# Performance work log

Hardware: AMD Instinct MI355X
Metric: run time of the kernel (lower is better)

## Reference

```python
import jax, jax.numpy as jnp
from jax import lax
import numpy as np


def _conv(x, w, b, groups=1):
    # x: NCHW, w: OIHW, stride 1, SAME padding
    y = lax.conv_general_dilated(x, w, (1, 1), 'SAME',
                                 dimension_numbers=('NCHW', 'OIHW', 'NCHW'),
                                 feature_group_count=groups)
    return y + b[None, :, None, None]


def setup_inputs() -> dict:
    key = jax.random.key(0)
    ks = jax.random.split(key, 9)
    B, C, H, W, N, K = 8, 64, 256, 256, 10, 64
    f = lambda k, s, sc=0.05: jax.random.normal(k, s, dtype=jnp.float32) * sc
    return dict(
        x=jax.random.normal(ks[0], (B, C, H, W), dtype=jnp.float32),
        ln_g=jnp.ones((C,), jnp.float32), ln_b=jnp.zeros((C,), jnp.float32),
        conv3_w=f(ks[1], (C, C, 3, 3)), conv3_b=jnp.zeros((C,), jnp.float32),
        dw_w=f(ks[2], (C, 1, 3, 3)), dw_b=jnp.zeros((C,), jnp.float32),
        c1_w=f(ks[3], (C, C, 1, 1)), c1_b=jnp.zeros((C,), jnp.float32),
        c2_w=f(ks[4], (N, C, 1, 1)), c2_b=jnp.zeros((N,), jnp.float32),
        base=f(ks[5], (N, K, K), 1.0),
        up_w=f(ks[6], (K, C, 3, 3)), up_b=jnp.zeros((K,), jnp.float32),
        down_w=f(ks[7], (C, K, 3, 3)), down_b=jnp.zeros((C,), jnp.float32),
    )


def reference(x, ln_g, ln_b, conv3_w, conv3_b, dw_w, dw_b, c1_w, c1_b,
              c2_w, c2_b, base, up_w, up_b, down_w, down_b):
    eps = 1e-5
    # LayerNorm over channel dim (permute(0,2,3,1) -> LN(last) -> permute back)
    mu = jnp.mean(x, axis=1, keepdims=True)
    var = jnp.var(x, axis=1, keepdims=True)
    xn = (x - mu) / jnp.sqrt(var + eps) * ln_g[None, :, None, None] + ln_b[None, :, None, None]
    x1 = jax.nn.gelu(_conv(xn, conv3_w, conv3_b), approximate=False)
    # predict module: dwconv -> GAP -> 1x1 -> relu -> 1x1 -> softmax over N
    C = x.shape[1]
    p = _conv(x1, dw_w, dw_b, groups=C)
    p = jnp.mean(p, axis=(2, 3), keepdims=True)           # [B,C,1,1]
    p = jax.nn.relu(_conv(p, c1_w, c1_b))
    p = _conv(p, c2_w, c2_b)[:, :, 0, 0]                  # [B,N]
    w = jax.nn.softmax(p, axis=1)                         # [B,N]
    # blend N basis KxK matrices per sample
    Wm = jnp.einsum('bn,nkl->bkl', w, base)               # [B,K,K]
    xm = _conv(x1, up_w, up_b)                            # [B,K,H,W]
    B, K, H, Wd = xm.shape
    xm = jnp.einsum('bkl,bkm->blm', Wm, xm.reshape(B, K, H * Wd)).reshape(B, K, H, Wd)
    xm = _conv(xm, down_w, down_b)                        # [B,C,H,W]
    return x + xm
```

## Files before the change

kernel.cpp:

```cpp
#include <hip/hip_runtime.h>
#include <math.h>

constexpr int B = 8, C = 64, H = 256, W = 256, HWc = H * W, N = 10;

typedef short bf8 __attribute__((ext_vector_type(8)));
typedef float f4  __attribute__((ext_vector_type(4)));
typedef unsigned short ushort;

__device__ __forceinline__ ushort f2bf(float f) {
  unsigned u = __builtin_bit_cast(unsigned, f);
  unsigned r = (u + 0x7fffu + ((u >> 16) & 1u)) >> 16;
  return (ushort)r;
}
__device__ __forceinline__ float bf2f(ushort h) {
  unsigned u = ((unsigned)h) << 16;
  return __builtin_bit_cast(float, u);
}

__global__ __launch_bounds__(256) void ln_k(
    const float* __restrict__ x, const float* __restrict__ g,
    const float* __restrict__ bt, ushort* __restrict__ xn) {
  int pix = blockIdx.x * 256 + threadIdx.x;
  int b = blockIdx.y;
  const float* xp = x + (size_t)b * C * HWc + pix;
  float v[64];
  float s = 0.f, s2 = 0.f;
#pragma unroll
  for (int c = 0; c < 64; c++) {
    v[c] = xp[(size_t)c * HWc];
    s += v[c]; s2 += v[c] * v[c];
  }
  float mu = s * (1.f / 64);
  float var = s2 * (1.f / 64) - mu * mu;
  float rstd = rsqrtf(var + 1e-5f);
  ushort* op = xn + ((size_t)b * HWc + pix) * 64;
#pragma unroll
  for (int ch = 0; ch < 8; ch++) {
    union { ushort us[8]; int4 v4; } pk;
#pragma unroll
    for (int j = 0; j < 8; j++) {
      int c = ch * 8 + j;
      pk.us[j] = f2bf((v[c] - mu) * rstd * g[c] + bt[c]);
    }
    *reinterpret_cast<int4*>(op + ch * 8) = pk.v4;
  }
}

__global__ void prep_w(const float* __restrict__ w3, const float* __restrict__ wu,
                       const float* __restrict__ wd, ushort* __restrict__ frags) {
  int idx = blockIdx.x * 256 + threadIdx.x;
  if (idx >= 3 * 4608) return;
  int conv = idx / 4608, r = idx % 4608;
  int s = r >> 8, cf = (r >> 6) & 3, lane = r & 63;
  const float* w = (conv == 0) ? w3 : (conv == 1) ? wu : wd;
  int co = (cf << 4) + (lane & 15);
  int tap = s >> 1;
  ushort* o = frags + conv * 36864 + ((size_t)r) * 8;
#pragma unroll
  for (int j = 0; j < 8; j++) {
    int ci = ((s & 1) << 5) + ((lane >> 4) << 3) + j;
    o[j] = f2bf(w[(co * 64 + ci) * 9 + tap]);
  }
}

typedef __attribute__((address_space(3))) unsigned lds_u32;
typedef __attribute__((address_space(1))) const unsigned glb_u32;

__device__ __forceinline__ void stage_gll(
    char* ldsbuf, const ushort* __restrict__ in, const ushort* __restrict__ zbuf,
    int b, int h0, int w0, int ch2, int tid) {
  int wave = tid >> 6, lane = tid & 63;
#pragma unroll
  for (int it = 0; it < 6; it++) {
    int idx = it * 256 + wave * 64 + lane;
    int pix = idx >> 2, ch = idx & 3;
    int r = pix / 18, c = pix % 18;
    int gh = h0 + r - 1, gw = w0 + c - 1;
    int chs = ch ^ ((c >> 1) & 3);
    bool ok = (idx < 1296) && (gh >= 0) && (gh < H) && (gw >= 0) && (gw < W);
    const ushort* src = ok
        ? in + (((size_t)b * H + gh) * W + gw) * 64 + ch2 * 32 + chs * 8
        : zbuf;
    char* dst = ldsbuf + (it * 256 + wave * 64) * 16;
    __builtin_amdgcn_global_load_lds((glb_u32*)(const void*)src,
                                     (lds_u32*)(void*)dst, 16, 0, 0);
  }
}

__device__ __forceinline__ void compute_half(
    const char* lds, const bf8* __restrict__ wf, int ch2,
    int wave, int lm, int lk, f4 (&acc)[16]) {
#pragma unroll
  for (int dx = 0; dx < 3; dx++) {
    bf8 wb3[3];
#pragma unroll
    for (int dy = 0; dy < 3; dy++) {
      int s = ((dy * 3 + dx) << 1) | ch2;
      wb3[dy] = wf[(s * 4 + wave) * 64 + (lk << 4) + lm];
    }
    int lc = lm + dx;
    int swz = ((lc >> 1) & 3) << 4;
#pragma unroll
    for (int hf = 0; hf < 2; hf++) {
      bf8 a[10];
#pragma unroll
      for (int r = 0; r < 10; r++) {
        int row = hf * 8 + r;
        int off = (((row * 18 + lc) << 6) + (lk << 4)) ^ swz;
        a[r] = *reinterpret_cast<const bf8*>(lds + off);
      }
#pragma unroll
      for (int dy = 0; dy < 3; dy++)
#pragma unroll
        for (int f = 0; f < 8; f++)
          acc[hf * 8 + f] =
              __builtin_amdgcn_mfma_f32_16x16x32_bf16(a[f + dy], wb3[dy], acc[hf * 8 + f], 0, 0, 0);
    }
  }
}

#define STAGE_PIPELINE(bufA_, bufB_)                                      \
  stage_gll(bufA_, in, zbuf, b, h0, w0, 0, tid);                          \
  stage_gll(bufB_, in, zbuf, b, h0, w0, 1, tid);                          \
  asm volatile("s_waitcnt vmcnt(6)" ::: "memory");                        \
  __builtin_amdgcn_s_barrier();                                           \
  __builtin_amdgcn_sched_barrier(0);                                      \
  compute_half(bufA_, wf, 0, wave, lm, lk, acc);                          \
  asm volatile("s_waitcnt vmcnt(0)" ::: "memory");                        \
  __builtin_amdgcn_s_barrier();                                           \
  __builtin_amdgcn_sched_barrier(0);                                      \
  compute_half(bufB_, wf, 1, wave, lm, lk, acc);

__device__ __forceinline__ void red_at(
    float* ldsf, const float (&a)[8], float* __restrict__ Ssum,
    int b, int tid) {
  __syncthreads();
#pragma unroll
  for (int j = 0; j < 8; j++) ldsf[j * 256 + tid] = a[j];
  __syncthreads();
  if (tid < 64) {
    float s = 0.f;
#pragma unroll
    for (int kk = 0; kk < 32; kk++) s += ldsf[(tid & 7) * 256 + kk * 8 + (tid >> 3)];
    atomicAdd(&Ssum[b * 64 + tid], s);
  }
}

template <int ACT, int OM, int DOST>
__global__ __launch_bounds__(256, 2) void conv_mfma(
    const ushort* __restrict__ in, const ushort* __restrict__ wfrag,
    const float* __restrict__ bias, const float* __restrict__ resid,
    ushort* __restrict__ outb, float* __restrict__ outf,
    float* __restrict__ Ssum, const ushort* __restrict__ zbuf) {
  __shared__ char lds[2 * 24576];
  char* ldsA = lds;
  char* ldsB = lds + 24576;
  int tid = threadIdx.x;
  int b = blockIdx.z;
  int h0 = blockIdx.y * 16, w0 = blockIdx.x * 16;
  int wave = tid >> 6, lane = tid & 63;
  int lm = lane & 15, lk = lane >> 4;
  const bf8* wf = reinterpret_cast<const bf8*>(wfrag);

  f4 acc[16];
  {
    float bv = bias[(wave << 4) + lm];
    f4 ini = {bv, bv, bv, bv};
#pragma unroll
    for (int f = 0; f < 16; f++) acc[f] = ini;
  }

  STAGE_PIPELINE(ldsA, ldsB)

  float* ldsf = reinterpret_cast<float*>(lds);
  if (OM == 0) {
    float s8[8];
    if (DOST) {
#pragma unroll
      for (int j = 0; j < 8; j++) s8[j] = 0.f;
    }
    for (int h2 = 0; h2 < 2; h2++) {
      __syncthreads();
#pragma unroll
      for (int fr = 0; fr < 8; fr++) {
        int f = h2 * 8 + fr;
        int co = (wave << 4) + lm;
#pragma unroll
        for (int r = 0; r < 4; r++) {
          int p = (lk << 2) + r;
          ldsf[fr * 1024 + p * 64 + (co ^ ((p & 12) << 2))] = acc[f][r];
        }
      }
      __syncthreads();
#pragma unroll
      for (int i = 0; i < 4; i++) {
        int q2 = i * 256 + tid;
        int co8 = q2 & 7, p = (q2 >> 3) & 15, fr = q2 >> 7;
        int cb = (co8 * 8) ^ ((p & 12) << 2);
        f4 v0 = *reinterpret_cast<f4*>(&ldsf[fr * 1024 + p * 64 + cb]);
        f4 v1 = *reinterpret_cast<f4*>(&ldsf[fr * 1024 + p * 64 + cb + 4]);
        float vv[8] = {v0[0], v0[1], v0[2], v0[3], v1[0], v1[1], v1[2], v1[3]};
        union { ushort us[8]; int4 i4; } pk;
#pragma unroll
        for (int j = 0; j < 8; j++) {
          float v = vv[j];
          if (ACT) v = 0.5f * v * (1.f + erff(v * 0.70710678118654752f));
          if (DOST) s8[j] += v;
          pk.us[j] = f2bf(v);
        }
        *reinterpret_cast<int4*>(
            outb + (((size_t)b * H + h0 + h2 * 8 + fr) * W + w0 + p) * 64 + co8 * 8) = pk.i4;
      }
    }
    if (DOST) red_at(ldsf, s8, Ssum, b, tid);
  } else {
    for (int h2 = 0; h2 < 2; h2++) {
      __syncthreads();
      if ((wave >> 1) == h2) {
        int co32 = ((wave & 1) << 4) + lm;
#pragma unroll
        for (int f = 0; f < 16; f++) {
          int pxl = (f << 4) + (lk << 2);
          int pxs = pxl ^ ((co32 & 7) << 2);
          *reinterpret_cast<f4*>(&ldsf[co32 * 256 + pxs]) = acc[f];
        }
      }
      float4 rv[8];
#pragma unroll
      for (int i = 0; i < 8; i++) {
        int q2 = i * 256 + tid;
        int chunk = q2 & 63, co32 = q2 >> 6;
        int pq = chunk * 4;
        int co = h2 * 32 + co32;
        size_t o = ((size_t)(b * 64 + co)) * HWc +
                   (size_t)(h0 + (pq >> 4)) * W + w0 + (pq & 15);
        rv[i] = *reinterpret_cast<const float4*>(resid + o);
      }
      __syncthreads();
#pragma unroll
      for (int i = 0; i < 8; i++) {
        int q2 = i * 256 + tid;
        int chunk = q2 & 63, co32 = q2 >> 6;
        int pq = chunk * 4;
        int pxs = pq ^ ((co32 & 7) << 2);
        f4 v = *reinterpret_cast<f4*>(&ldsf[co32 * 256 + pxs]);
        int co = h2 * 32 + co32;
        size_t o = ((size_t)(b * 64 + co)) * HWc +
                   (size_t)(h0 + (pq >> 4)) * W + w0 + (pq & 15);
        float4 ov;
        ov.x = v[0] + rv[i].x; ov.y = v[1] + rv[i].y;
        ov.z = v[2] + rv[i].z; ov.w = v[3] + rv[i].w;
        *reinterpret_cast<float4*>(outf + o) = ov;
      }
    }
  }
}

__global__ __launch_bounds__(256, 2) void upmix_mfma(
    const ushort* __restrict__ in, const ushort* __restrict__ wfrag,
    const float* __restrict__ bias, const ushort* __restrict__ wmf,
    ushort* __restrict__ out, const ushort* __restrict__ zbuf) {
  __shared__ char ldsS[24576];
  __shared__ char ldsX[32768];
  int tid = threadIdx.x;
  int b = blockIdx.z;
  int h0 = blockIdx.y * 16, w0 = blockIdx.x * 16;
  int wave = tid >> 6, lane = tid & 63;
  int lm = lane & 15, lk = lane >> 4;
  const bf8* wf = reinterpret_cast<const bf8*>(wfrag);

  const bf8* wmb = reinterpret_cast<const bf8*>(wmf + (size_t)b * 4096);
  bf8 wm[2];
#pragma unroll
  for (int s = 0; s < 2; s++) wm[s] = wmb[(s * 4 + wave) * 64 + lane];

  f4 acc[16];
  {
    float bv = bias[(wave << 4) + lm];
    f4 ini = {bv, bv, bv, bv};
#pragma unroll
    for (int f = 0; f < 16; f++) acc[f] = ini;
  }

  STAGE_PIPELINE(ldsS, ldsX)
  __syncthreads();

#pragma unroll
  for (int f = 0; f < 16; f++) {
#pragma unroll
    for (int r = 0; r < 4; r++) {
      int pc = (lk << 2) + r;
      int pix = (f << 4) + pc;
      int off = ((pix << 7) + ((wave << 4) + lm) * 2) ^ ((pc & 7) << 4);
      *reinterpret_cast<ushort*>(ldsX + off) = f2bf(acc[f][r]);
    }
  }
  __syncthreads();

  f4 acc2[16];
#pragma unroll
  for (int f = 0; f < 16; f++) acc2[f] = (f4){0.f, 0.f, 0.f, 0.f};
#pragma unroll
  for (int s = 0; s < 2; s++) {
    int kbyte = ((s << 5) + (lk << 3)) << 1;
#pragma unroll
    for (int f = 0; f < 16; f++) {
      int off = ((((f << 4) + lm) << 7) + kbyte) ^ ((lm & 7) << 4);
      bf8 a = *reinterpret_cast<const bf8*>(ldsX + off);
      acc2[f] = __builtin_amdgcn_mfma_f32_16x16x32_bf16(a, wm[s], acc2[f], 0, 0, 0);
    }
  }

  float* ldsf = reinterpret_cast<float*>(ldsX);
  for (int h2 = 0; h2 < 2; h2++) {
    __syncthreads();
#pragma unroll
    for (int fr = 0; fr < 8; fr++) {
      int f = h2 * 8 + fr;
      int co = (wave << 4) + lm;
#pragma unroll
      for (int r = 0; r < 4; r++) {
        int p = (lk << 2) + r;
        ldsf[fr * 1024 + p * 64 + (co ^ ((p & 12) << 2))] = acc2[f][r];
      }
    }
    __syncthreads();
#pragma unroll
    for (int i = 0; i < 4; i++) {
      int q2 = i * 256 + tid;
      int co8 = q2 & 7, p = (q2 >> 3) & 15, fr = q2 >> 7;
      int cb = (co8 * 8) ^ ((p & 12) << 2);
      f4 v0 = *reinterpret_cast<f4*>(&ldsf[fr * 1024 + p * 64 + cb]);
      f4 v1 = *reinterpret_cast<f4*>(&ldsf[fr * 1024 + p * 64 + cb + 4]);
      float vv[8] = {v0[0], v0[1], v0[2], v0[3], v1[0], v1[1], v1[2], v1[3]};
      union { ushort us[8]; int4 i4; } pk;
#pragma unroll
      for (int j = 0; j < 8; j++) pk.us[j] = f2bf(vv[j]);
      *reinterpret_cast<int4*>(
          out + (((size_t)b * H + h0 + h2 * 8 + fr) * W + w0 + p) * 64 + co8 * 8) = pk.i4;
    }
  }
}

__global__ __launch_bounds__(256) void mlp_k(
    const ushort* __restrict__ x1, const float* __restrict__ Ssum,
    const float* __restrict__ dww, const float* __restrict__ dwb,
    const float* __restrict__ c1w, const float* __restrict__ c1b,
    const float* __restrict__ c2w, const float* __restrict__ c2b,
    const float* __restrict__ basep, ushort* __restrict__ wmf) {
  int b = blockIdx.x;
  int t = threadIdx.x;
  __shared__ float red[256];
  __shared__ float eg[4][64], corn[4][64];
  __shared__ float pm[64], p1[64], p2[16];
  const size_t bb = (size_t)b * HWc * 64;
#pragma unroll
  for (int st = 0; st < 4; st++) {
    float s = 0.f;
    for (int i = 0; i < 64; i++) {
      int idx = i * 256 + t;
      int pix = idx >> 6, c = idx & 63;
      size_t off;
      if (st == 0)      off = ((size_t)pix) * 64 + c;
      else if (st == 1) off = ((size_t)(H - 1) * W + pix) * 64 + c;
      else if (st == 2) off = ((size_t)pix * W) * 64 + c;
      else              off = ((size_t)pix * W + (W - 1)) * 64 + c;
      s += bf2f(x1[bb + off]);
    }
    red[t] = s;
    __syncthreads();
    if (t < 64) eg[st][t] = red[t] + red[t + 64] + red[t + 128] + red[t + 192];
    __syncthreads();
  }
  if (t < 64) {
    corn[0][t] = bf2f(x1[bb + t]);
    corn[1][t] = bf2f(x1[bb + ((size_t)(W - 1)) * 64 + t]);
    corn[2][t] = bf2f(x1[bb + ((size_t)(H - 1) * W) * 64 + t]);
    corn[3][t] = bf2f(x1[bb + ((size_t)(H - 1) * W + W - 1) * 64 + t]);
  }
  __syncthreads();
  if (t < 64) {
    float S = Ssum[b * 64 + t];
    float R0 = eg[0][t], Rh = eg[1][t], C0 = eg[2][t], Cw = eg[3][t];
    float X00 = corn[0][t], X0w = corn[1][t], Xh0 = corn[2][t], Xhw = corn[3][t];
    float acc = 0.f;
#pragma unroll
    for (int ky = 0; ky < 3; ky++)
#pragma unroll
      for (int kx = 0; kx < 3; kx++) {
        float T = S;
        if (ky == 2) T -= R0;
        if (ky == 0) T -= Rh;
        if (kx == 2) T -= C0;
        if (kx == 0) T -= Cw;
        if (ky == 2 && kx == 2) T += X00;
        if (ky == 2 && kx == 0) T += X0w;
        if (ky == 0 && kx == 2) T += Xh0;
        if (ky == 0 && kx == 0) T += Xhw;
        acc += dww[t * 9 + ky * 3 + kx] * T;
      }
    pm[t] = acc * (1.f / HWc) + dwb[t];
  }
  __syncthreads();
  if (t < 64) {
    float a = c1b[t];
    for (int ci = 0; ci < 64; ci++) a += pm[ci] * c1w[t * 64 + ci];
    p1[t] = fmaxf(a, 0.f);
  }
  __syncthreads();
  if (t < N) {
    float a2 = c2b[t];
    for (int ci = 0; ci < 64; ci++) a2 += p1[ci] * c2w[t * 64 + ci];
    p2[t] = a2;
  }
  __syncthreads();
  float m = -1e30f;
  for (int n = 0; n < N; n++) m = fmaxf(m, p2[n]);
  float ev[N], s = 0.f;
  for (int n = 0; n < N; n++) { ev[n] = expf(p2[n] - m); s += ev[n]; }
  float inv = 1.f / s;
  for (int idx = t; idx < 4096; idx += 256) {
    int j = idx & 7, lane = (idx >> 3) & 63, cf = (idx >> 9) & 3, s2 = idx >> 11;
    int k = (s2 << 5) + ((lane >> 4) << 3) + j;
    int l = (cf << 4) + (lane & 15);
    float acc = 0.f;
    for (int n = 0; n < N; n++) acc += ev[n] * inv * basep[n * 4096 + k * 64 + l];
    wmf[(size_t)b * 4096 + idx] = f2bf(acc);
  }
}

__global__ void zero_k(float* p, int n) {
  int i = blockIdx.x * 256 + threadIdx.x;
  if (i < n) p[i] = 0.f;
}

extern "C" void kernel_launch(void* const* d_in, const int* in_sizes, int n_in,
                              void* d_out, int out_size, void* d_ws, size_t ws_size,
                              hipStream_t stream) {
  const float* x       = (const float*)d_in[0];
  const float* ln_g    = (const float*)d_in[1];
  const float* ln_b    = (const float*)d_in[2];
  const float* conv3_w = (const float*)d_in[3];
  const float* conv3_b = (const float*)d_in[4];
  const float* dw_w    = (const float*)d_in[5];
  const float* dw_b    = (const float*)d_in[6];
  const float* c1_w    = (const float*)d_in[7];
  const float* c1_b    = (const float*)d_in[8];
  const float* c2_w    = (const float*)d_in[9];
  const float* c2_b    = (const float*)d_in[10];
  const float* basep   = (const float*)d_in[11];
  const float* up_w    = (const float*)d_in[12];
  const float* up_b    = (const float*)d_in[13];
  const float* down_w  = (const float*)d_in[14];
  const float* down_b  = (const float*)d_in[15];
  float* out = (float*)d_out;

  char* wsb = (char*)d_ws;
  size_t big = (size_t)B * HWc * 64 * sizeof(ushort);
  ushort* bufA   = (ushort*)wsb;
  ushort* bufB   = (ushort*)(wsb + big);
  ushort* wfrags = (ushort*)(wsb + 2 * big);
  ushort* wmfrag = (ushort*)(wsb + 2 * big + 3 * 36864 * 2);
  float*  Ssum   = (float*)(wsb + 2 * big + 3 * 36864 * 2 + 8 * 4096 * 2);
  const ushort* zbuf = (const ushort*)(Ssum + 512);

  prep_w<<<54, 256, 0, stream>>>(conv3_w, up_w, down_w, wfrags);
  zero_k<<<8, 256, 0, stream>>>(Ssum, 2048);
  ln_k<<<dim3(HWc / 256, B), 256, 0, stream>>>(x, ln_g, ln_b, bufA);
  conv_mfma<1, 0, 1><<<dim3(16, 16, B), 256, 0, stream>>>(
      bufA, wfrags + 0 * 36864, conv3_b, nullptr, bufB, nullptr, Ssum, zbuf);
  mlp_k<<<B, 256, 0, stream>>>(bufB, Ssum, dw_w, dw_b, c1_w, c1_b, c2_w, c2_b,
                               basep, wmfrag);
  upmix_mfma<<<dim3(16, 16, B), 256, 0, stream>>>(
      bufB, wfrags + 1 * 36864, up_b, wmfrag, bufA, zbuf);
  conv_mfma<0, 1, 0><<<dim3(16, 16, B), 256, 0, stream>>>(
      bufA, wfrags + 2 * 36864, down_b, x, nullptr, out, Ssum, zbuf);
}
```

Measured before the change: 302.7 us.

## Process four row tiles per conv block with cross-tile prefetch and register-resident weights

Each conv block now walks four vertically stacked 16x16 tiles. The next tile's halo is staged into LDS while the current tile finishes compute and its epilogue, and all 18 weight fragments are held in registers instead of being reloaded per tap. The epilogue gets its own LDS region so staging can overlap it, and the residual loads for the down conv are issued before staging. This is meant to hide global-load latency and cut repeated weight fetches and launch-tail effects. The costs are more registers and 64KB of LDS per block, which may lower occupancy, and a grid four times smaller.

```diff
diff --git a/kernel.cpp b/kernel.cpp
--- a/kernel.cpp
+++ b/kernel.cpp
@@ -15,6 +15,18 @@
 __device__ __forceinline__ float bf2f(ushort h) {
   unsigned u = ((unsigned)h) << 16;
   return __builtin_bit_cast(float, u);
+}
+
+template <int NN>
+__device__ __forceinline__ void vm_gate() {
+  asm volatile("s_waitcnt vmcnt(%0)" :: "i"(NN) : "memory");
+  __builtin_amdgcn_s_barrier();
+  __builtin_amdgcn_sched_barrier(0);
+}
+__device__ __forceinline__ void bar_lds() {
+  asm volatile("s_waitcnt lgkmcnt(0)" ::: "memory");
+  __builtin_amdgcn_s_barrier();
+  __builtin_amdgcn_sched_barrier(0);
 }
 
 __global__ __launch_bounds__(256) void ln_k(
@@ -88,16 +100,10 @@
 }
 
 __device__ __forceinline__ void compute_half(
-    const char* lds, const bf8* __restrict__ wf, int ch2,
+    const char* lds, const bf8 (&wb)[18], int ch2,
     int wave, int lm, int lk, f4 (&acc)[16]) {
 #pragma unroll
   for (int dx = 0; dx < 3; dx++) {
-    bf8 wb3[3];
-#pragma unroll
-    for (int dy = 0; dy < 3; dy++) {
-      int s = ((dy * 3 + dx) << 1) | ch2;
-      wb3[dy] = wf[(s * 4 + wave) * 64 + (lk << 4) + lm];
-    }
     int lc = lm + dx;
     int swz = ((lc >> 1) & 3) << 4;
 #pragma unroll
@@ -110,26 +116,16 @@
         a[r] = *reinterpret_cast<const bf8*>(lds + off);
       }
 #pragma unroll
-      for (int dy = 0; dy < 3; dy++)
+      for (int dy = 0; dy < 3; dy++) {
+        int s = ((dy * 3 + dx) << 1) | ch2;
 #pragma unroll
         for (int f = 0; f < 8; f++)
           acc[hf * 8 + f] =
-              __builtin_amdgcn_mfma_f32_16x16x32_bf16(a[f + dy], wb3[dy], acc[hf * 8 + f], 0, 0, 0);
-    }
-  }
-}
-
-#define STAGE_PIPELINE(bufA_, bufB_)                                      \
-  stage_gll(bufA_, in, zbuf, b, h0, w0, 0, tid);                          \
-  stage_gll(bufB_, in, zbuf, b, h0, w0, 1, tid);                          \
-  asm volatile("s_waitcnt vmcnt(6)" ::: "memory");                        \
-  __builtin_amdgcn_s_barrier();                                           \
-  __builtin_amdgcn_sched_barrier(0);                                      \
-  compute_half(bufA_, wf, 0, wave, lm, lk, acc);                          \
-  asm volatile("s_waitcnt vmcnt(0)" ::: "memory");                        \
-  __builtin_amdgcn_s_barrier();                                           \
-  __builtin_amdgcn_sched_barrier(0);                                      \
-  compute_half(bufB_, wf, 1, wave, lm, lk, acc);
+              __builtin_amdgcn_mfma_f32_16x16x32_bf16(a[f + dy], wb[s], acc[hf * 8 + f], 0, 0, 0);
+      }
+    }
+  }
+}
 
 __device__ __forceinline__ void red_at(
     float* ldsf, const float (&a)[8], float* __restrict__ Ssum,
@@ -146,59 +142,69 @@
   }
 }
 
-template <int ACT, int OM, int DOST>
-__global__ __launch_bounds__(256, 2) void conv_mfma(
-    const ushort* __restrict__ in, const ushort* __restrict__ wfrag,
-    const float* __restrict__ bias, const float* __restrict__ resid,
-    ushort* __restrict__ outb, float* __restrict__ outf,
-    float* __restrict__ Ssum, const ushort* __restrict__ zbuf) {
-  __shared__ char lds[2 * 24576];
-  char* ldsA = lds;
-  char* ldsB = lds + 24576;
-  int tid = threadIdx.x;
-  int b = blockIdx.z;
-  int h0 = blockIdx.y * 16, w0 = blockIdx.x * 16;
-  int wave = tid >> 6, lane = tid & 63;
-  int lm = lane & 15, lk = lane >> 4;
-  const bf8* wf = reinterpret_cast<const bf8*>(wfrag);
-
+template <int ACT, int OM, int DOST, int T>
+__device__ __forceinline__ void conv_tile(
+    const ushort* __restrict__ in, const bf8 (&wb)[18], float bv,
+    const float* __restrict__ resid, ushort* __restrict__ outb,
+    float* __restrict__ outf, const ushort* __restrict__ zbuf,
+    char* ldsA, char* ldsB, float* epif, float (&s8)[8],
+    int b, int h0, int w0, int tid, int wave, int lm, int lk) {
+  constexpr bool NXT = (T < 3);
+  constexpr int GA = (T == 0) ? 6 : (OM ? 38 : 14);
+  constexpr int GB = OM ? (T == 0 ? 6 : (T == 3 ? 16 : 22))
+                        : (T == 0 ? 6 : (T == 3 ? 8 : 14));
   f4 acc[16];
   {
-    float bv = bias[(wave << 4) + lm];
     f4 ini = {bv, bv, bv, bv};
 #pragma unroll
     for (int f = 0; f < 16; f++) acc[f] = ini;
   }
 
-  STAGE_PIPELINE(ldsA, ldsB)
-
-  float* ldsf = reinterpret_cast<float*>(lds);
-  if (OM == 0) {
-    float s8[8];
-    if (DOST) {
-#pragma unroll
-      for (int j = 0; j < 8; j++) s8[j] = 0.f;
-    }
-    for (int h2 = 0; h2 < 2; h2++) {
-      __syncthreads();
-#pragma unroll
-      for (int fr = 0; fr < 8; fr++) {
-        int f = h2 * 8 + fr;
+  vm_gate<GA>();
+  compute_half(ldsA, wb, 0, wave, lm, lk, acc);
+  bar_lds();
+  if (NXT) stage_gll(ldsA, in, zbuf, b, h0 + 16, w0, 0, tid);
+  vm_gate<GB>();
+  compute_half(ldsB, wb, 1, wave, lm, lk, acc);
+  bar_lds();
+
+  float4 rv[16];
+  if constexpr (OM == 1) {
+#pragma unroll
+    for (int i = 0; i < 16; i++) {
+      int q = i >> 2;
+      int q2 = (i & 3) * 256 + tid;
+      int chunk = q2 & 63, co16 = q2 >> 6;
+      int pq = chunk * 4;
+      int co = q * 16 + co16;
+      size_t o = ((size_t)(b * 64 + co)) * HWc +
+                 (size_t)(h0 + (pq >> 4)) * W + w0 + (pq & 15);
+      rv[i] = *reinterpret_cast<const float4*>(resid + o);
+    }
+  }
+  if (NXT) stage_gll(ldsB, in, zbuf, b, h0 + 16, w0, 1, tid);
+
+  if constexpr (OM == 0) {
+#pragma unroll
+    for (int q = 0; q < 4; q++) {
+#pragma unroll
+      for (int fr = 0; fr < 4; fr++) {
+        int f = q * 4 + fr;
         int co = (wave << 4) + lm;
 #pragma unroll
         for (int r = 0; r < 4; r++) {
           int p = (lk << 2) + r;
-          ldsf[fr * 1024 + p * 64 + (co ^ ((p & 12) << 2))] = acc[f][r];
+          epif[fr * 1024 + p * 64 + (co ^ ((p & 12) << 2))] = acc[f][r];
         }
       }
-      __syncthreads();
-#pragma unroll
-      for (int i = 0; i < 4; i++) {
+      bar_lds();
+#pragma unroll
+      for (int i = 0; i < 2; i++) {
         int q2 = i * 256 + tid;
         int co8 = q2 & 7, p = (q2 >> 3) & 15, fr = q2 >> 7;
         int cb = (co8 * 8) ^ ((p & 12) << 2);
-        f4 v0 = *reinterpret_cast<f4*>(&ldsf[fr * 1024 + p * 64 + cb]);
-        f4 v1 = *reinterpret_cast<f4*>(&ldsf[fr * 1024 + p * 64 + cb + 4]);
+        f4 v0 = *reinterpret_cast<f4*>(&epif[fr * 1024 + p * 64 + cb]);
+        f4 v1 = *reinterpret_cast<f4*>(&epif[fr * 1024 + p * 64 + cb + 4]);
         float vv[8] = {v0[0], v0[1], v0[2], v0[3], v1[0], v1[1], v1[2], v1[3]};
         union { ushort us[8]; int4 i4; } pk;
 #pragma unroll
@@ -209,51 +215,83 @@
           pk.us[j] = f2bf(v);
         }
         *reinterpret_cast<int4*>(
-            outb + (((size_t)b * H + h0 + h2 * 8 + fr) * W + w0 + p) * 64 + co8 * 8) = pk.i4;
-      }
-    }
-    if (DOST) red_at(ldsf, s8, Ssum, b, tid);
+            outb + (((size_t)b * H + h0 + q * 4 + fr) * W + w0 + p) * 64 + co8 * 8) = pk.i4;
+      }
+      bar_lds();
+    }
   } else {
-    for (int h2 = 0; h2 < 2; h2++) {
-      __syncthreads();
-      if ((wave >> 1) == h2) {
-        int co32 = ((wave & 1) << 4) + lm;
+#pragma unroll
+    for (int q = 0; q < 4; q++) {
+      if (wave == q) {
 #pragma unroll
         for (int f = 0; f < 16; f++) {
           int pxl = (f << 4) + (lk << 2);
-          int pxs = pxl ^ ((co32 & 7) << 2);
-          *reinterpret_cast<f4*>(&ldsf[co32 * 256 + pxs]) = acc[f];
+          int pxs = pxl ^ ((lm & 7) << 2);
+          *reinterpret_cast<f4*>(&epif[lm * 256 + pxs]) = acc[f];
         }
       }
-      float4 rv[8];
-#pragma unroll
-      for (int i = 0; i < 8; i++) {
+      bar_lds();
+#pragma unroll
+      for (int i = 0; i < 4; i++) {
         int q2 = i * 256 + tid;
-        int chunk = q2 & 63, co32 = q2 >> 6;
+        int chunk = q2 & 63, co16 = q2 >> 6;
         int pq = chunk * 4;
-        int co = h2 * 32 + co32;
+        int pxs = pq ^ ((co16 & 7) << 2);
+        f4 v = *reinterpret_cast<f4*>(&epif[co16 * 256 + pxs]);
+        int co = q * 16 + co16;
         size_t o = ((size_t)(b * 64 + co)) * HWc +
                    (size_t)(h0 + (pq >> 4)) * W + w0 + (pq & 15);
-        rv[i] = *reinterpret_cast<const float4*>(resid + o);
-      }
-      __syncthreads();
-#pragma unroll
-      for (int i = 0; i < 8; i++) {
-        int q2 = i * 256 + tid;
-        int chunk = q2 & 63, co32 = q2 >> 6;
-        int pq = chunk * 4;
-        int pxs = pq ^ ((co32 & 7) << 2);
-        f4 v = *reinterpret_cast<f4*>(&ldsf[co32 * 256 + pxs]);
-        int co = h2 * 32 + co32;
-        size_t o = ((size_t)(b * 64 + co)) * HWc +
-                   (size_t)(h0 + (pq >> 4)) * W + w0 + (pq & 15);
+        float4 r = rv[q * 4 + i];
         float4 ov;
-        ov.x = v[0] + rv[i].x; ov.y = v[1] + rv[i].y;
-        ov.z = v[2] + rv[i].z; ov.w = v[3] + rv[i].w;
+        ov.x = v[0] + r.x; ov.y = v[1] + r.y; ov.z = v[2] + r.z; ov.w = v[3] + r.w;
         *reinterpret_cast<float4*>(outf + o) = ov;
       }
-    }
-  }
+      bar_lds();
+    }
+  }
+}
+
+template <int ACT, int OM, int DOST>
+__global__ __launch_bounds__(256, 2) void conv_mfma(
+    const ushort* __restrict__ in, const ushort* __restrict__ wfrag,
+    const float* __restrict__ bias, const float* __restrict__ resid,
+    ushort* __restrict__ outb, float* __restrict__ outf,
+    float* __restrict__ Ssum, const ushort* __restrict__ zbuf) {
+  __shared__ char lds[65536];
+  char* ldsA = lds;
+  char* ldsB = lds + 24576;
+  float* epif = reinterpret_cast<float*>(lds + 49152);
+  int tid = threadIdx.x;
+  int b = blockIdx.z;
+  int h0base = blockIdx.y * 64, w0 = blockIdx.x * 16;
+  int wave = tid >> 6, lane = tid & 63;
+  int lm = lane & 15, lk = lane >> 4;
+  const bf8* wf = reinterpret_cast<const bf8*>(wfrag);
+
+  bf8 wb[18];
+#pragma unroll
+  for (int s = 0; s < 18; s++) wb[s] = wf[(s * 4 + wave) * 64 + (lk << 4) + lm];
+  float bv = bias[(wave << 4) + lm];
+
+  float s8[8];
+  if (DOST) {
+#pragma unroll
+    for (int j = 0; j < 8; j++) s8[j] = 0.f;
+  }
+
+  stage_gll(ldsA, in, zbuf, b, h0base, w0, 0, tid);
+  stage_gll(ldsB, in, zbuf, b, h0base, w0, 1, tid);
+
+  conv_tile<ACT, OM, DOST, 0>(in, wb, bv, resid, outb, outf, zbuf, ldsA, ldsB,
+                              epif, s8, b, h0base +  0, w0, tid, wave, lm, lk);
+  conv_tile<ACT, OM, DOST, 1>(in, wb, bv, resid, outb, outf, zbuf, ldsA, ldsB,
+                              epif, s8, b, h0base + 16, w0, tid, wave, lm, lk);
+  conv_tile<ACT, OM, DOST, 2>(in, wb, bv, resid, outb, outf, zbuf, ldsA, ldsB,
+                              epif, s8, b, h0base + 32, w0, tid, wave, lm, lk);
+  conv_tile<ACT, OM, DOST, 3>(in, wb, bv, resid, outb, outf, zbuf, ldsA, ldsB,
+                              epif, s8, b, h0base + 48, w0, tid, wave, lm, lk);
+
+  if (DOST) red_at(epif, s8, Ssum, b, tid);
 }
 
 __global__ __launch_bounds__(256, 2) void upmix_mfma(
@@ -269,6 +307,9 @@
   int lm = lane & 15, lk = lane >> 4;
   const bf8* wf = reinterpret_cast<const bf8*>(wfrag);
 
+  bf8 wb[18];
+#pragma unroll
+  for (int s = 0; s < 18; s++) wb[s] = wf[(s * 4 + wave) * 64 + (lk << 4) + lm];
   const bf8* wmb = reinterpret_cast<const bf8*>(wmf + (size_t)b * 4096);
   bf8 wm[2];
 #pragma unroll
@@ -282,8 +323,13 @@
     for (int f = 0; f < 16; f++) acc[f] = ini;
   }
 
-  STAGE_PIPELINE(ldsS, ldsX)
-  __syncthreads();
+  stage_gll(ldsS, in, zbuf, b, h0, w0, 0, tid);
+  stage_gll(ldsX, in, zbuf, b, h0, w0, 1, tid);
+  vm_gate<6>();
+  compute_half(ldsS, wb, 0, wave, lm, lk, acc);
+  vm_gate<0>();
+  compute_half(ldsX, wb, 1, wave, lm, lk, acc);
+  bar_lds();
 
 #pragma unroll
   for (int f = 0; f < 16; f++) {
@@ -295,7 +341,7 @@
       *reinterpret_cast<ushort*>(ldsX + off) = f2bf(acc[f][r]);
     }
   }
-  __syncthreads();
+  bar_lds();
 
   f4 acc2[16];
 #pragma unroll
@@ -313,7 +359,7 @@
 
   float* ldsf = reinterpret_cast<float*>(ldsX);
   for (int h2 = 0; h2 < 2; h2++) {
-    __syncthreads();
+    bar_lds();
 #pragma unroll
     for (int fr = 0; fr < 8; fr++) {
       int f = h2 * 8 + fr;
@@ -324,7 +370,7 @@
         ldsf[fr * 1024 + p * 64 + (co ^ ((p & 12) << 2))] = acc2[f][r];
       }
     }
-    __syncthreads();
+    bar_lds();
 #pragma unroll
     for (int i = 0; i < 4; i++) {
       int q2 = i * 256 + tid;
@@ -467,12 +513,12 @@
   prep_w<<<54, 256, 0, stream>>>(conv3_w, up_w, down_w, wfrags);
   zero_k<<<8, 256, 0, stream>>>(Ssum, 2048);
   ln_k<<<dim3(HWc / 256, B), 256, 0, stream>>>(x, ln_g, ln_b, bufA);
-  conv_mfma<1, 0, 1><<<dim3(16, 16, B), 256, 0, stream>>>(
+  conv_mfma<1, 0, 1><<<dim3(16, 4, B), 256, 0, stream>>>(
       bufA, wfrags + 0 * 36864, conv3_b, nullptr, bufB, nullptr, Ssum, zbuf);
   mlp_k<<<B, 256, 0, stream>>>(bufB, Ssum, dw_w, dw_b, c1_w, c1_b, c2_w, c2_b,
                                basep, wmfrag);
   upmix_mfma<<<dim3(16, 16, B), 256, 0, stream>>>(
       bufB, wfrags + 1 * 36864, up_b, wmfrag, bufA, zbuf);
-  conv_mfma<0, 1, 0><<<dim3(16, 16, B), 256, 0, stream>>>(
+  conv_mfma<0, 1, 0><<<dim3(16, 4, B), 256, 0, stream>>>(
       bufA, wfrags + 2 * 36864, down_b, x, nullptr, out, Ssum, zbuf);
 }
```

New measurement: 489.4 us. 61.7% more time.
